# Performance work log

Hardware: AMD Instinct MI355X
Metric: run time of the kernel (lower is better)

Reference implementation:

```python
import jax, jax.numpy as jnp
import numpy as np

N = 50000          # num nodes
E = 800000         # num edges (avg degree 16)
D_IN = 128         # input_size
H = 128            # hidden_size
BN_EPS = 1e-5


def setup_inputs() -> dict:
    key = jax.random.key(0)
    ks = jax.random.split(key, 16)
    std = 1.0 / np.sqrt(H)
    u = lambda k, shape: jax.random.uniform(k, shape, jnp.float32, -std, std)
    return {
        "x": jax.random.normal(ks[0], (N, D_IN), jnp.float32),
        "hx": jax.random.normal(ks[1], (N, H), jnp.float32),
        "cx": jax.random.normal(ks[2], (N, H), jnp.float32),
        "edge_src": jax.random.randint(ks[3], (E,), 0, N, jnp.int32),
        "edge_dst": jax.random.randint(ks[4], (E,), 0, N, jnp.int32),
        "edge_weight": jax.random.uniform(ks[5], (E,), jnp.float32) / 16.0,  # ~normalized adj values
        "gcn_weight": u(ks[6], (D_IN, H)),
        "bias": u(ks[7], (H,)),
        "x2h_w": u(ks[8], (4 * H, H)),
        "x2h_b": u(ks[9], (4 * H,)),
        "h2h_w": u(ks[10], (4 * H, H)),
        "h2h_b": u(ks[11], (4 * H,)),
        "bn_gamma": u(ks[12], (H,)),
        "bn_beta": u(ks[13], (H,)),
        "bn_mean": jnp.zeros((H,), jnp.float32),
        "bn_var": jnp.ones((H,), jnp.float32),
    }


def reference(x, hx, cx, edge_src, edge_dst, edge_weight, gcn_weight, bias,
              x2h_w, x2h_b, h2h_w, h2h_b, bn_gamma, bn_beta, bn_mean, bn_var):
    # GCN: support = x @ W, then sparse adj @ support via gather/segment-sum
    support = x @ gcn_weight                                   # (N, H)
    msgs = edge_weight[:, None] * support[edge_src]            # (E, H)
    agg = jax.ops.segment_sum(msgs, edge_dst, num_segments=N)  # (N, H) = spmm(adj, support)
    h = jax.nn.relu(agg)
    # dropout: eval mode -> identity
    h = h + bias
    # BatchNorm1d (eval mode, running stats)
    h = (h - bn_mean) * jax.lax.rsqrt(bn_var + BN_EPS) * bn_gamma + bn_beta
    # fused LSTM gates: x2h(h) + h2h(hx)
    gates = h @ x2h_w.T + x2h_b + hx @ h2h_w.T + h2h_b         # (N, 4H)
    i_g, f_g, g_g, o_g = jnp.split(gates, 4, axis=1)
    cy = cx * jax.nn.sigmoid(f_g) + jax.nn.sigmoid(i_g) * jnp.tanh(g_g)
    hy = jax.nn.sigmoid(o_g) * jnp.tanh(cy)
    return hy, cy
```

## Files before the change

### kernel.cpp

```cpp
#include <hip/hip_runtime.h>

#define NN 50000
#define NE 800000
#define HH 128
#define BN_EPS 1e-5f
#define SCAN_NB ((NN + 255) / 256)

typedef unsigned short u16;
typedef unsigned int u32;
typedef short bf16x8 __attribute__((ext_vector_type(8)));
typedef float f32x4 __attribute__((ext_vector_type(4)));

static __device__ __forceinline__ float bf2f(u16 u){
  union { u32 i; float f; } v; v.i = ((u32)u) << 16; return v.f;
}
static __device__ __forceinline__ u16 f2bf(float f){
  union { float f; u32 i; } v; v.f = f;
  u32 x = v.i;
  return (u16)((x + 0x7fffu + ((x >> 16) & 1u)) >> 16);
}
static __device__ __forceinline__ float sigm(float x){
  return 1.f / (1.f + __expf(-x));
}
static __device__ __forceinline__ float tanh_fast(float x){
  return 1.f - 2.f / (1.f + __expf(2.f * x));
}


__global__ void zero_kernel(int* __restrict__ p, int n){
  int i = blockIdx.x * blockDim.x + threadIdx.x;
  if (i < n) p[i] = 0;
}

__global__ void hist_kernel(const int* __restrict__ dst, int* __restrict__ counts, int E){
  int e = blockIdx.x * blockDim.x + threadIdx.x;
  if (e < E) atomicAdd(&counts[dst[e]], 1);
}


__global__ __launch_bounds__(256) void scan_bsum(
    const int* __restrict__ counts, int* __restrict__ bsums, int n){
  int i = blockIdx.x * 256 + threadIdx.x;
  int v = (i < n) ? counts[i] : 0;
#pragma unroll
  for (int off = 1; off < 64; off <<= 1) v += __shfl_xor(v, off);
  __shared__ int ws[4];
  if ((threadIdx.x & 63) == 0) ws[threadIdx.x >> 6] = v;
  __syncthreads();
  if (threadIdx.x == 0) bsums[blockIdx.x] = ws[0] + ws[1] + ws[2] + ws[3];
}

__global__ __launch_bounds__(256) void scan_tops(int* __restrict__ bsums, int nb){
  __shared__ int sh[256];
  int t = threadIdx.x;
  int v = (t < nb) ? bsums[t] : 0;
  sh[t] = v;
  __syncthreads();
  for (int off = 1; off < 256; off <<= 1){
    int u = (t >= off) ? sh[t - off] : 0;
    __syncthreads();
    sh[t] += u;
    __syncthreads();
  }
  if (t < nb) bsums[t] = sh[t] - v;
}

__global__ __launch_bounds__(256) void scan_final(
    const int* __restrict__ counts, const int* __restrict__ bsums,
    int* __restrict__ offs, int* __restrict__ cursor, int n){
  __shared__ int sh[256];
  int t = threadIdx.x;
  int i = blockIdx.x * 256 + t;
  int v = (i < n) ? counts[i] : 0;
  sh[t] = v;
  __syncthreads();
  for (int off = 1; off < 256; off <<= 1){
    int u = (t >= off) ? sh[t - off] : 0;
    __syncthreads();
    sh[t] += u;
    __syncthreads();
  }
  int excl = sh[t] - v + bsums[blockIdx.x];
  if (i < n){ offs[i] = excl; cursor[i] = excl; }
}

__global__ void scatter_kernel(const int* __restrict__ src, const int* __restrict__ dst,
                               const float* __restrict__ w, int* __restrict__ cursor,
                               int2* __restrict__ esw, int E){
  int e = blockIdx.x * blockDim.x + threadIdx.x;
  if (e < E){
    int d = dst[e];
    int pos = atomicAdd(&cursor[d], 1);
    esw[pos] = make_int2(src[e], __float_as_int(w[e]));
  }
}

__global__ void prep_pack(const float* __restrict__ x2hw, const float* __restrict__ h2hw,
                          const float* __restrict__ x2hb, const float* __restrict__ h2hb,
                          const float* __restrict__ gcnw,
                          u16* __restrict__ wcat, u16* __restrict__ wgcn,
                          float* __restrict__ bsum){
  int i = blockIdx.x * blockDim.x + threadIdx.x;
  int n = i >> 8, k = i & 255;
  float v = (k < 128) ? x2hw[n * 128 + k] : h2hw[n * 128 + (k - 128)];
  int nt = n >> 4, lc = n & 15;
  int kk = k >> 5, lq = (k >> 3) & 3, e = k & 7;
  wcat[(((nt * 8 + kk) * 64) + lq * 16 + lc) * 8 + e] = f2bf(v);
  if (i < 16384){
    int nn = i >> 7, kx = i & 127;
    wgcn[i] = f2bf(gcnw[kx * 128 + nn]);
  }
  if (i < 512) bsum[i] = x2hb[i] + h2hb[i];
}

__global__ __launch_bounds__(256) void support_mfma(
    const float* __restrict__ x, const u16* __restrict__ wgcn,
    u16* __restrict__ support, int N){
  int tid = threadIdx.x;
  int wave = tid >> 6, lane = tid & 63;
  int c = lane & 15, q = lane >> 4;
  int row0 = blockIdx.x * 64 + wave * 16;
  int arow = row0 + c; if (arow > N - 1) arow = N - 1;
  f32x4 acc[8];
#pragma unroll
  for (int t = 0; t < 8; t++) acc[t] = (f32x4){0.f, 0.f, 0.f, 0.f};

  const u16* wp = wgcn + (size_t)c * 128 + q * 8;
#pragma unroll
  for (int k0 = 0; k0 < 128; k0 += 32){
    const float* ap = x + (size_t)arow * 128 + k0 + q * 8;
    float4 f0 = *(const float4*)ap;
    float4 f1 = *(const float4*)(ap + 4);
    u16 tmp[8] = {f2bf(f0.x), f2bf(f0.y), f2bf(f0.z), f2bf(f0.w),
                  f2bf(f1.x), f2bf(f1.y), f2bf(f1.z), f2bf(f1.w)};
    bf16x8 afrag = *(bf16x8*)tmp;
#pragma unroll
    for (int t = 0; t < 8; t++){
      bf16x8 bfrag = *(const bf16x8*)(wp + (size_t)t * 16 * 128 + k0);
      acc[t] = __builtin_amdgcn_mfma_f32_16x16x32_bf16(afrag, bfrag, acc[t], 0, 0, 0);
    }
  }
#pragma unroll
  for (int t = 0; t < 8; t++){
#pragma unroll
    for (int j = 0; j < 4; j++){
      int r = row0 + q * 4 + j;
      if (r < N) support[(size_t)r * 128 + t * 16 + c] = f2bf(acc[t][j]);
    }
  }
}

__global__ __launch_bounds__(256) void agg_bn2(
    const u16* __restrict__ support, const int2* __restrict__ esw,
    const int* __restrict__ offs, const int* __restrict__ counts,
    const float* __restrict__ bias, const float* __restrict__ gamma,
    const float* __restrict__ beta, const float* __restrict__ mean,
    const float* __restrict__ var, const float* __restrict__ hx,
    u16* __restrict__ hbn, u16* __restrict__ hxb, int N){
  int wid = blockIdx.x * 4 + (threadIdx.x >> 6);
  int lane = threadIdx.x & 63;
  if (wid >= N) return;
  int c = lane * 2;
  float2 hv = *(const float2*)(hx + (size_t)wid * HH + c);
  int start = offs[wid];
  int deg   = counts[wid];
  float a0 = 0.f, a1 = 0.f;
  for (int base = 0; base < deg; base += 64){
    int cnt = deg - base; if (cnt > 64) cnt = 64;
    int2 my = make_int2(0, 0);
    if (lane < cnt) my = esw[start + base + lane];
    int e = 0;
    for (; e + 8 <= cnt; e += 8){
      int s[8]; float g[8]; u32 u[8];
#pragma unroll
      for (int k = 0; k < 8; k++){
        s[k] = __shfl(my.x, e + k);
        g[k] = __int_as_float(__shfl(my.y, e + k));
      }
#pragma unroll
      for (int k = 0; k < 8; k++)
        u[k] = *(const u32*)(support + (size_t)s[k] * HH + c);
#pragma unroll
      for (int k = 0; k < 8; k++){
        a0 = fmaf(g[k], bf2f((u16)(u[k] & 0xffffu)), a0);
        a1 = fmaf(g[k], bf2f((u16)(u[k] >> 16)), a1);
      }
    }
    for (; e + 4 <= cnt; e += 4){
      int s[4]; float g[4]; u32 u[4];
#pragma unroll
      for (int k = 0; k < 4; k++){
        s[k] = __shfl(my.x, e + k);
        g[k] = __int_as_float(__shfl(my.y, e + k));
      }
#pragma unroll
      for (int k = 0; k < 4; k++)
        u[k] = *(const u32*)(support + (size_t)s[k] * HH + c);
#pragma unroll
      for (int k = 0; k < 4; k++){
        a0 = fmaf(g[k], bf2f((u16)(u[k] & 0xffffu)), a0);
        a1 = fmaf(g[k], bf2f((u16)(u[k] >> 16)), a1);
      }
    }
    for (; e < cnt; e++){
      int   si = __shfl(my.x, e);
      float gi = __int_as_float(__shfl(my.y, e));
      u32 ui = *(const u32*)(support + (size_t)si * HH + c);
      a0 = fmaf(gi, bf2f((u16)(ui & 0xffffu)), a0);
      a1 = fmaf(gi, bf2f((u16)(ui >> 16)), a1);
    }
  }
  float h0 = fmaxf(a0, 0.f) + bias[c];
  float h1 = fmaxf(a1, 0.f) + bias[c + 1];
  float s0 = gamma[c]     * rsqrtf(var[c]     + BN_EPS);
  float s1 = gamma[c + 1] * rsqrtf(var[c + 1] + BN_EPS);
  float r0 = (h0 - mean[c])     * s0 + beta[c];
  float r1 = (h1 - mean[c + 1]) * s1 + beta[c + 1];
  u32 pack = (u32)f2bf(r0) | ((u32)f2bf(r1) << 16);
  *(u32*)(hbn + (size_t)wid * HH + c) = pack;
  u32 hp = (u32)f2bf(hv.x) | ((u32)f2bf(hv.y) << 16);
  *(u32*)(hxb + (size_t)wid * HH + c) = hp;
}

__global__ __launch_bounds__(1024) void gates_mfma4(
    const u16* __restrict__ hbn, const u16* __restrict__ hxb,
    const u16* __restrict__ wcat, const float* __restrict__ bsum,
    const float* __restrict__ cx, float* __restrict__ out, int N){
  __shared__ bf16x8 lds_b[8192];
  int tid = threadIdx.x;
  int wave = tid >> 6, lane = tid & 63;
  int c = lane & 15, q = lane >> 4;
  int rb = wave >> 2, cg = wave & 3;
  int hc = blockIdx.y;
  int hloc = hc * 64 + cg * 16 + c;

  const bf16x8* wsrc = (const bf16x8*)wcat;
#pragma unroll
  for (int it = 0; it < 8; it++){
    int idx = it * 1024 + tid;
    int lf = idx >> 6, l = idx & 63;
    int scg = lf >> 5, sg = (lf >> 3) & 3, skk = lf & 7;
    int nt = sg * 8 + hc * 4 + scg;
    lds_b[idx] = wsrc[(nt * 8 + skk) * 64 + l];
  }
  __syncthreads();

  float bi  = bsum[hloc];
  float bf_ = bsum[128 + hloc];
  float bg  = bsum[256 + hloc];
  float bo  = bsum[384 + hloc];
  const size_t NH = (size_t)N * HH;

  const int nchunk = (N + 127) >> 7;
  for (int chunk = blockIdx.x; chunk < nchunk; chunk += gridDim.x){
    int rowbase = chunk * 128 + rb * 32;
    f32x4 acc[2][4];
#pragma unroll
    for (int b = 0; b < 2; b++)
#pragma unroll
      for (int g = 0; g < 4; g++) acc[b][g] = (f32x4){0.f, 0.f, 0.f, 0.f};
    int ar0 = rowbase + c;      if (ar0 > N - 1) ar0 = N - 1;
    int ar1 = rowbase + 16 + c; if (ar1 > N - 1) ar1 = N - 1;

#pragma unroll
    for (int kk = 0; kk < 8; kk++){
      const u16* abase = ((kk < 4) ? (hbn + (size_t)(kk * 32))
                                   : (hxb + (size_t)((kk - 4) * 32))) + q * 8;
      bf16x8 a0 = *(const bf16x8*)(abase + (size_t)ar0 * 128);
      bf16x8 a1 = *(const bf16x8*)(abase + (size_t)ar1 * 128);
#pragma unroll
      for (int g = 0; g < 4; g++){
        bf16x8 bfrag = lds_b[((cg * 4 + g) * 8 + kk) * 64 + lane];
        acc[0][g] = __builtin_amdgcn_mfma_f32_16x16x32_bf16(a0, bfrag, acc[0][g], 0, 0, 0);
        acc[1][g] = __builtin_amdgcn_mfma_f32_16x16x32_bf16(a1, bfrag, acc[1][g], 0, 0, 0);
      }
    }
#pragma unroll
    for (int b = 0; b < 2; b++){
#pragma unroll
      for (int j = 0; j < 4; j++){
        int r = rowbase + b * 16 + q * 4 + j;
        if (r < N){
          float gi = acc[b][0][j] + bi;
          float gf = acc[b][1][j] + bf_;
          float gg = acc[b][2][j] + bg;
          float go = acc[b][3][j] + bo;
          float is = sigm(gi), fs = sigm(gf), gt = tanh_fast(gg), os = sigm(go);
          float co = cx[(size_t)r * HH + hloc];
          float cyv = co * fs + is * gt;
          out[(size_t)r * HH + hloc]      = os * tanh_fast(cyv);
          out[NH + (size_t)r * HH + hloc] = cyv;
        }
      }
    }
  }
}


extern "C" void kernel_launch(void* const* d_in, const int* in_sizes, int n_in,
                              void* d_out, int out_size, void* d_ws, size_t ws_size,
                              hipStream_t stream){
  const float* x     = (const float*)d_in[0];
  const float* hx    = (const float*)d_in[1];
  const float* cx    = (const float*)d_in[2];
  const int*   esrc  = (const int*)d_in[3];
  const int*   edst  = (const int*)d_in[4];
  const float* ew    = (const float*)d_in[5];
  const float* gcn_w = (const float*)d_in[6];
  const float* bias  = (const float*)d_in[7];
  const float* x2hw  = (const float*)d_in[8];
  const float* x2hb  = (const float*)d_in[9];
  const float* h2hw  = (const float*)d_in[10];
  const float* h2hb  = (const float*)d_in[11];
  const float* bn_g  = (const float*)d_in[12];
  const float* bn_b  = (const float*)d_in[13];
  const float* bn_m  = (const float*)d_in[14];
  const float* bn_v  = (const float*)d_in[15];
  float* out = (float*)d_out;

  char* w = (char*)d_ws;
  u16* support = (u16*)w; w += (((size_t)NN * HH * 2) + 255) & ~(size_t)255;
  u16* hbn     = (u16*)w; w += (((size_t)NN * HH * 2) + 255) & ~(size_t)255;
  u16* hxb     = (u16*)w; w += (((size_t)NN * HH * 2) + 255) & ~(size_t)255;
  int* counts  = (int*)w; w += (((size_t)NN * 4) + 255) & ~(size_t)255;
  int* offs    = (int*)w; w += (((size_t)NN * 4) + 255) & ~(size_t)255;
  int* cursor  = (int*)w; w += (((size_t)NN * 4) + 255) & ~(size_t)255;
  int* bsums   = (int*)w; w += (((size_t)SCAN_NB * 4) + 255) & ~(size_t)255;
  int2* esw    = (int2*)w; w += (((size_t)NE * 8) + 255) & ~(size_t)255;
  u16* wcat    = (u16*)w; w += (((size_t)512 * 256 * 2) + 255) & ~(size_t)255;
  u16* wgcn    = (u16*)w; w += (((size_t)128 * 128 * 2) + 255) & ~(size_t)255;
  float* bsum  = (float*)w; w += (((size_t)512 * 4) + 255) & ~(size_t)255;

  prep_pack<<<512, 256, 0, stream>>>(x2hw, h2hw, x2hb, h2hb, gcn_w, wcat, wgcn, bsum);
  zero_kernel<<<(NN + 255) / 256, 256, 0, stream>>>(counts, NN);
  hist_kernel<<<(NE + 255) / 256, 256, 0, stream>>>(edst, counts, NE);
  scan_bsum<<<SCAN_NB, 256, 0, stream>>>(counts, bsums, NN);
  scan_tops<<<1, 256, 0, stream>>>(bsums, SCAN_NB);
  scan_final<<<SCAN_NB, 256, 0, stream>>>(counts, bsums, offs, cursor, NN);
  scatter_kernel<<<(NE + 255) / 256, 256, 0, stream>>>(esrc, edst, ew, cursor, esw, NE);
  support_mfma<<<(NN + 63) / 64, 256, 0, stream>>>(x, wgcn, support, NN);
  agg_bn2<<<(NN + 3) / 4, 256, 0, stream>>>(support, esw, offs, counts,
                                            bias, bn_g, bn_b, bn_m, bn_v, hx, hbn, hxb, NN);
  gates_mfma4<<<dim3(128, 2), 1024, 0, stream>>>(hbn, hxb, wcat, bsum, cx, out, NN);
}
```

Before: 404.1 us.

## Keep gate weights in registers and split K across wave halves with LDS reduction

The gates kernel is restructured so each wave holds its B weight tiles in registers instead of LDS. Sixteen waves split the K dimension in two: one half uses hbn and the other uses hxb. Partial sums are combined through a double-buffered LDS exchange with one __syncthreads per 16-row chunk. This drops the per-iteration LDS weight reads and the 2D grid. The costs are heavy register pressure, a block barrier per chunk, and only half the waves running the epilogue. The chunk count assumes N is a multiple of 16.

```diff
diff --git a/kernel.cpp b/kernel.cpp
--- a/kernel.cpp
+++ b/kernel.cpp
@@ -222,77 +222,74 @@
   *(u32*)(hxb + (size_t)wid * HH + c) = hp;
 }
 
-__global__ __launch_bounds__(1024) void gates_mfma4(
+__global__ __launch_bounds__(1024, 1) void gates_mfma5(
     const u16* __restrict__ hbn, const u16* __restrict__ hxb,
     const u16* __restrict__ wcat, const float* __restrict__ bsum,
     const float* __restrict__ cx, float* __restrict__ out, int N){
-  __shared__ bf16x8 lds_b[8192];
+  __shared__ float lbuf[2][8][16][64];
   int tid = threadIdx.x;
   int wave = tid >> 6, lane = tid & 63;
   int c = lane & 15, q = lane >> 4;
-  int rb = wave >> 2, cg = wave & 3;
-  int hc = blockIdx.y;
-  int hloc = hc * 64 + cg * 16 + c;
+  int cw = wave & 7, kh = wave >> 3;
+  int hloc = cw * 16 + c;
 
   const bf16x8* wsrc = (const bf16x8*)wcat;
-#pragma unroll
-  for (int it = 0; it < 8; it++){
-    int idx = it * 1024 + tid;
-    int lf = idx >> 6, l = idx & 63;
-    int scg = lf >> 5, sg = (lf >> 3) & 3, skk = lf & 7;
-    int nt = sg * 8 + hc * 4 + scg;
-    lds_b[idx] = wsrc[(nt * 8 + skk) * 64 + l];
-  }
-  __syncthreads();
-
-  float bi  = bsum[hloc];
-  float bf_ = bsum[128 + hloc];
-  float bg  = bsum[256 + hloc];
-  float bo  = bsum[384 + hloc];
+  bf16x8 btile[4][4];
+#pragma unroll
+  for (int g = 0; g < 4; g++)
+#pragma unroll
+    for (int kk = 0; kk < 4; kk++)
+      btile[g][kk] = wsrc[((size_t)((g * 8 + cw) * 8) + kh * 4 + kk) * 64 + lane];
+
+  float bi = 0.f, bf_ = 0.f, bg = 0.f, bo = 0.f;
+  if (kh == 0){
+    bi  = bsum[hloc];
+    bf_ = bsum[128 + hloc];
+    bg  = bsum[256 + hloc];
+    bo  = bsum[384 + hloc];
+  }
+  const u16* abuf = kh ? hxb : hbn;
   const size_t NH = (size_t)N * HH;
-
-  const int nchunk = (N + 127) >> 7;
+  const int nchunk = N >> 4;
+  int p = 0;
+
   for (int chunk = blockIdx.x; chunk < nchunk; chunk += gridDim.x){
-    int rowbase = chunk * 128 + rb * 32;
-    f32x4 acc[2][4];
-#pragma unroll
-    for (int b = 0; b < 2; b++)
-#pragma unroll
-      for (int g = 0; g < 4; g++) acc[b][g] = (f32x4){0.f, 0.f, 0.f, 0.f};
-    int ar0 = rowbase + c;      if (ar0 > N - 1) ar0 = N - 1;
-    int ar1 = rowbase + 16 + c; if (ar1 > N - 1) ar1 = N - 1;
-
-#pragma unroll
-    for (int kk = 0; kk < 8; kk++){
-      const u16* abase = ((kk < 4) ? (hbn + (size_t)(kk * 32))
-                                   : (hxb + (size_t)((kk - 4) * 32))) + q * 8;
-      bf16x8 a0 = *(const bf16x8*)(abase + (size_t)ar0 * 128);
-      bf16x8 a1 = *(const bf16x8*)(abase + (size_t)ar1 * 128);
-#pragma unroll
-      for (int g = 0; g < 4; g++){
-        bf16x8 bfrag = lds_b[((cg * 4 + g) * 8 + kk) * 64 + lane];
-        acc[0][g] = __builtin_amdgcn_mfma_f32_16x16x32_bf16(a0, bfrag, acc[0][g], 0, 0, 0);
-        acc[1][g] = __builtin_amdgcn_mfma_f32_16x16x32_bf16(a1, bfrag, acc[1][g], 0, 0, 0);
-      }
-    }
-#pragma unroll
-    for (int b = 0; b < 2; b++){
+    int row0 = chunk << 4;
+    f32x4 acc[4];
+#pragma unroll
+    for (int g = 0; g < 4; g++) acc[g] = (f32x4){0.f, 0.f, 0.f, 0.f};
+    const u16* ap = abuf + (size_t)(row0 + c) * 128 + q * 8;
+#pragma unroll
+    for (int kk = 0; kk < 4; kk++){
+      bf16x8 a = *(const bf16x8*)(ap + kk * 32);
+#pragma unroll
+      for (int g = 0; g < 4; g++)
+        acc[g] = __builtin_amdgcn_mfma_f32_16x16x32_bf16(a, btile[g][kk], acc[g], 0, 0, 0);
+    }
+    if (kh == 1){
+#pragma unroll
+      for (int g = 0; g < 4; g++)
+#pragma unroll
+        for (int j = 0; j < 4; j++)
+          lbuf[p][cw][g * 4 + j][lane] = acc[g][j];
+    }
+    __syncthreads();
+    if (kh == 0){
 #pragma unroll
       for (int j = 0; j < 4; j++){
-        int r = rowbase + b * 16 + q * 4 + j;
-        if (r < N){
-          float gi = acc[b][0][j] + bi;
-          float gf = acc[b][1][j] + bf_;
-          float gg = acc[b][2][j] + bg;
-          float go = acc[b][3][j] + bo;
-          float is = sigm(gi), fs = sigm(gf), gt = tanh_fast(gg), os = sigm(go);
-          float co = cx[(size_t)r * HH + hloc];
-          float cyv = co * fs + is * gt;
-          out[(size_t)r * HH + hloc]      = os * tanh_fast(cyv);
-          out[NH + (size_t)r * HH + hloc] = cyv;
-        }
-      }
-    }
+        int r = row0 + q * 4 + j;
+        float gi = acc[0][j] + lbuf[p][cw][0 + j][lane]  + bi;
+        float gf = acc[1][j] + lbuf[p][cw][4 + j][lane]  + bf_;
+        float gg = acc[2][j] + lbuf[p][cw][8 + j][lane]  + bg;
+        float go = acc[3][j] + lbuf[p][cw][12 + j][lane] + bo;
+        float is = sigm(gi), fs = sigm(gf), gt = tanh_fast(gg), os = sigm(go);
+        float co = cx[(size_t)r * HH + hloc];
+        float cyv = co * fs + is * gt;
+        out[(size_t)r * HH + hloc]      = os * tanh_fast(cyv);
+        out[NH + (size_t)r * HH + hloc] = cyv;
+      }
+    }
+    p ^= 1;
   }
 }
 
@@ -341,5 +338,5 @@
   support_mfma<<<(NN + 63) / 64, 256, 0, stream>>>(x, wgcn, support, NN);
   agg_bn2<<<(NN + 3) / 4, 256, 0, stream>>>(support, esw, offs, counts,
                                             bias, bn_g, bn_b, bn_m, bn_v, hx, hbn, hxb, NN);
-  gates_mfma4<<<dim3(128, 2), 1024, 0, stream>>>(hbn, hxb, wcat, bsum, cx, out, NN);
-}
+  gates_mfma5<<<256, 1024, 0, stream>>>(hbn, hxb, wcat, bsum, cx, out, NN);
+}
```

Result: faster. 350.0 us (-13.4%).
